# Performance work log

Measured on AMD Instinct MI355X. Metric: run time of the kernel, lower is better.

The kernel has to match this reference:

```python
import jax, jax.numpy as jnp
import numpy as np

B, C, S = 4, 512, 8192   # batch, channels, seq len
E = 256                  # q_dim // r1 = projected dim
D = 256                  # dilaion: block size; window width = 2*D (D even)


def setup_inputs() -> dict:
    key = jax.random.key(0)
    ks = jax.random.split(key, 6)
    w = 0.05
    return {
        "x1": jax.random.normal(ks[0], (B, C, S), jnp.float32),
        "mask": jnp.ones((B, 1, S), jnp.float32),
        "Wq": jax.random.normal(ks[1], (E, C), jnp.float32) * w,
        "bq": jnp.zeros((E,), jnp.float32),
        "Wk": jax.random.normal(ks[2], (E, C), jnp.float32) * w,
        "bk": jnp.zeros((E,), jnp.float32),
        "Wv": jax.random.normal(ks[3], (E, C), jnp.float32) * w,
        "bv": jnp.zeros((E,), jnp.float32),
        "Wo": jax.random.normal(ks[4], (C, E), jnp.float32) * w,
        "bo": jnp.zeros((C,), jnp.float32),
    }


def _windows(x, nb, d):
    # x: [B, ch, S] -> nb overlapping windows of width 2d (stride d, halo d//2 each side)
    b, ch, _ = x.shape
    xp = jnp.pad(x, ((0, 0), (0, 0), (d // 2, d // 2)))  # [B, ch, S + d]
    lo = xp[:, :, : nb * d].reshape(b, ch, nb, d)
    hi = xp[:, :, d:].reshape(b, ch, nb, d)
    return jnp.concatenate([lo, hi], axis=-1).transpose(0, 2, 1, 3)  # [B, nb, ch, 2d]


def reference(x1, mask, Wq, bq, Wk, bk, Wv, bv, Wo, bo):
    nb = S // D  # S divisible by D -> no tail padding branch
    # 1x1 conv projections
    q = jnp.einsum('ec,bcs->bes', Wq, x1) + bq[None, :, None]
    k = jnp.einsum('ec,bcs->bes', Wk, x1) + bk[None, :, None]
    v = jnp.einsum('ec,bcs->bes', Wv, x1) + bv[None, :, None]

    qw = q.reshape(B, E, nb, D).transpose(0, 2, 1, 3)   # [B, nb, E, D]
    kw = _windows(k, nb, D)                              # [B, nb, E, 2D]
    vw = _windows(v, nb, D)                              # [B, nb, E, 2D]
    pm = mask[:, 0:1, :]                                 # padding mask [B,1,S]
    pmw = _windows(pm, nb, D)                            # [B, nb, 1, 2D]

    W = 2 * D
    # original loop `window_mask[:, :, i:i+D] = 1 for i in range(D)` -> union covers
    # columns [0, 2D-2]; only the last column stays 0 (rows identical)
    win = (jnp.arange(W) < W - 1).astype(jnp.float32)    # [2D]
    fmask = win[None, None, None, :] * pmw               # [B, nb, 1, 2D]

    energy = jnp.einsum('bneq,bnek->bnqk', qw, kw) / np.float32(np.sqrt(E))
    attn = jax.nn.softmax(energy + jnp.log(fmask + 1e-6), axis=-1) * fmask
    out = jnp.einsum('bnek,bnqk->bneq', vw, attn)        # [B, nb, E, D]

    h = jax.nn.gelu(out, approximate=False)
    h = jnp.einsum('oe,bneq->bnoq', Wo, h) + bo[None, None, :, None]  # [B, nb, C, D]
    y = h.transpose(0, 2, 1, 3).reshape(B, C, nb * D)[:, :, :S]
    return y * mask[:, 0:1, :]
```

## Files before the change

kernel.cpp:

```cpp
#include <hip/hip_runtime.h>
#include <hip/hip_bf16.h>

typedef __attribute__((ext_vector_type(8))) short short8;
typedef __attribute__((ext_vector_type(4))) float f32x4;
typedef __attribute__((ext_vector_type(4))) int int4v;

#define DI __device__ __forceinline__

constexpr int Bq = 4, Cc = 512, Ss = 8192, Ee = 256;
constexpr int SP = 8448;
constexpr long XSLAB = 4194304;

DI unsigned short f2bf(float f) {
    unsigned int u = __float_as_uint(f);
    unsigned int r = u + 0x7fffu + ((u >> 16) & 1u);
    return (unsigned short)(r >> 16);
}

union U16x8 { int4v v; unsigned short u[8]; };

DI void gll16(const void* g, void* l) {
    __builtin_amdgcn_global_load_lds(
        (const __attribute__((address_space(1))) unsigned int*)g,
        (__attribute__((address_space(3))) unsigned int*)l, 16, 0, 0);
}

DI unsigned pkbf(float lo, float hi) {
    unsigned r;
    asm("v_cvt_pk_bf16_f32 %0, %1, %2" : "=v"(r) : "v"(lo), "v"(hi));
    return r;
}

DI short8 mk8(unsigned a, unsigned b, unsigned c, unsigned d) {
    int4v v; v[0] = (int)a; v[1] = (int)b; v[2] = (int)c; v[3] = (int)d;
    union { int4v i; short8 s; } U; U.i = v; return U.s;
}

DI f32x4 max4(f32x4 a, f32x4 b) {
    f32x4 r;
    r[0] = fmaxf(a[0], b[0]); r[1] = fmaxf(a[1], b[1]);
    r[2] = fmaxf(a[2], b[2]); r[3] = fmaxf(a[3], b[3]);
    return r;
}

DI float gelu_t(float x) {
    float x2 = x * x;
    float z = x * (0.7978845608f + 0.0356774081f * x2);
    float az = fabsf(z);
    float e = __expf(-2.f * az);
    float th = (1.f - e) / (1.f + e);
    th = (z < 0.f) ? -th : th;
    return 0.5f * x * (1.f + th);
}

DI int SIG(int k)  { return ((k & 4) << 2) | ((k & 24) >> 1) | (k & 3); }
DI int SIG2(int k) { return SIG(SIG(k)); }

__global__ __launch_bounds__(256) void kprep(
    const float* __restrict__ Wq, const float* __restrict__ Wk, const float* __restrict__ Wv,
    const float* __restrict__ Wo, unsigned short* __restrict__ Wqkv_b, unsigned short* __restrict__ Wo_b,
    unsigned short* __restrict__ kTp, unsigned short* __restrict__ vp)
{
    int blk = blockIdx.x, t = threadIdx.x;
    if (blk < 1536) {
        int i = blk * 256 + t;
        if (i < 768 * 512) {
            int m = i >> 9, c = i & 511;
            const float* src = (m < 256) ? Wq : ((m < 512) ? Wk : Wv);
            Wqkv_b[i] = f2bf(src[(m & 255) * 512 + c]);
        }
        if (i < 512 * 256) {
            int kap = i & 255;
            int src = (i & ~255) | (kap & ~31) | SIG(kap & 31);
            Wo_b[i] = f2bf(Wo[src]);
        }
    } else {
        int i = (blk - 1536) * 256 + t;
        int4v z = {0, 0, 0, 0};
        if (i < 32768) {
            int b = i >> 13, r = i & 8191;
            int side = r >> 12, off = r & 4095;
            *(int4v*)(kTp + (long)b * SP * 256 + (long)(side ? 8320 : 0) * 256 + off * 8) = z;
        } else {
            int j = i - 32768;
            int b = j >> 13, r = j & 8191;
            int row = r >> 5, side = (r >> 4) & 1, sc = r & 15;
            *(int4v*)(vp + ((long)b * 256 + row) * SP + side * 8320 + sc * 8) = z;
        }
    }
}

__global__ __launch_bounds__(256) void ktr_x(const float* __restrict__ x1g, unsigned short* __restrict__ xT4)
{
    const float* x1b = x1g + (long)blockIdx.y * Cc * Ss;
    unsigned short* xT = xT4 + (long)blockIdx.y * XSLAB;
    __shared__ unsigned short tile[64][72];
    int t = threadIdx.x;
    int bs = blockIdx.x & 127, bc = blockIdx.x >> 7;
    int s0 = bs * 64, c0 = bc * 64;
    int cl = t >> 4, sl = (t & 15) * 4;
    for (int it = 0; it < 4; ++it) {
        int c = cl + it * 16;
        float4 vv = *(const float4*)(x1b + (long)(c0 + c) * Ss + s0 + sl);
        tile[c][sl + 0] = f2bf(vv.x);
        tile[c][sl + 1] = f2bf(vv.y);
        tile[c][sl + 2] = f2bf(vv.z);
        tile[c][sl + 3] = f2bf(vv.w);
    }
    __syncthreads();
    int s_loc = t >> 2, cseg = (t & 3) * 16;
    for (int half = 0; half < 2; ++half) {
        U16x8 u;
        for (int j = 0; j < 8; ++j) u.u[j] = tile[cseg + half * 8 + j][s_loc];
        *(int4v*)(xT + (long)(s0 + s_loc) * Cc + c0 + cseg + half * 8) = u.v;
    }
}

__global__ __launch_bounds__(256) void kqkv(
    const unsigned short* __restrict__ xT4, const unsigned short* __restrict__ Wqkv,
    const float* __restrict__ bq, const float* __restrict__ bk, const float* __restrict__ bv,
    unsigned short* __restrict__ qT, unsigned short* __restrict__ kTp, unsigned short* __restrict__ vp,
    int b0)
{
    __shared__ int4v As[1024], Bs[1024];
    int b = b0 + blockIdx.y;
    const unsigned short* xT = xT4 + (long)blockIdx.y * XSLAB;
    int wg = blockIdx.x;
    int type = wg >> 7, id = wg & 127;
    const unsigned short *A, *Bt; unsigned short* Op;
    long opitch; const float* bias; bool biasRow;
    if (type < 2) {
        int mt = id >> 1, nt = id & 1;
        A  = xT + (long)(mt * 128) * 512;
        Bt = Wqkv + (long)(type * 256 + nt * 128) * 512;
        if (type == 0)
            Op = qT + (long)b * Ss * Ee + (long)(mt * 128) * Ee + nt * 128;
        else
            Op = kTp + (long)b * SP * Ee + (long)(128 + mt * 128) * Ee + nt * 128;
        opitch = Ee;
        bias = (type ? bk : bq) + nt * 128;
        biasRow = false;
    } else {
        int mt = id >> 6, nt = id & 63;
        A  = Wqkv + (long)(512 + mt * 128) * 512;
        Bt = xT + (long)(nt * 128) * 512;
        Op = vp + (long)b * Ee * SP + (long)(mt * 128) * SP + 128 + nt * 128;
        opitch = SP;
        bias = bv + mt * 128;
        biasRow = true;
    }
    int t = threadIdx.x, lane = t & 63, wv = t >> 6;
    int wr = (wv >> 1) * 64, wc = (wv & 1) * 64;

    int soff[4];
    #pragma unroll
    for (int i = 0; i < 4; ++i) {
        int seg = t + 256 * i, row = seg >> 3, cs = seg & 7;
        soff[i] = row * 512 + ((cs ^ (row & 7)) * 8);
    }
    char* adst = (char*)As + wv * 1024;
    char* bdst = (char*)Bs + wv * 1024;

    f32x4 acc[4][4] = {};
    for (int kk = 0; kk < 8; ++kk) {
        #pragma unroll
        for (int i = 0; i < 4; ++i) {
            gll16(A  + soff[i] + kk * 64, adst + i * 4096);
            gll16(Bt + soff[i] + kk * 64, bdst + i * 4096);
        }
        asm volatile("s_waitcnt vmcnt(0)" ::: "memory");
        __syncthreads();
        for (int ks = 0; ks < 2; ++ks) {
            int csk = ks * 4 + (lane >> 4);
            short8 af[4], bfr[4];
            #pragma unroll
            for (int mi = 0; mi < 4; ++mi) {
                int m = wr + mi * 16 + (lane & 15);
                af[mi] = *(const short8*)&As[m * 8 + (csk ^ (m & 7))];
            }
            #pragma unroll
            for (int ni = 0; ni < 4; ++ni) {
                int nn = wc + ni * 16 + (lane & 15);
                bfr[ni] = *(const short8*)&Bs[nn * 8 + (csk ^ (nn & 7))];
            }
            #pragma unroll
            for (int mi = 0; mi < 4; ++mi)
                #pragma unroll
                for (int ni = 0; ni < 4; ++ni)
                    acc[mi][ni] = __builtin_amdgcn_mfma_f32_16x16x32_bf16(af[mi], bfr[ni], acc[mi][ni], 0, 0, 0);
        }
        __syncthreads();
    }
    for (int mi = 0; mi < 4; ++mi)
        for (int ni = 0; ni < 4; ++ni) {
            int mrow = wr + mi * 16 + ((lane >> 4) * 4);
            int ncol = wc + ni * 16 + (lane & 15);
            int nc2 = biasRow ? ((ncol & ~31) | SIG2(ncol & 31)) : ncol;
            for (int r = 0; r < 4; ++r) {
                float bval = biasRow ? bias[mrow + r] : bias[ncol];
                Op[(long)(mrow + r) * opitch + nc2] = f2bf(acc[mi][ni][r] + bval);
            }
        }
}

__global__ __launch_bounds__(512, 1) void kattn(
    const unsigned short* __restrict__ qT, const unsigned short* __restrict__ kTp,
    const unsigned short* __restrict__ vp,  const unsigned short* __restrict__ Wo_b,
    const float* __restrict__ mask, const float* __restrict__ bo,
    float* __restrict__ y)
{
    __shared__ __align__(16) char SH[137216];
    float* fmaskL = (float*)(SH + 131072);
    float* l2maskL = (float*)(SH + 133120);
    float* boL    = (float*)(SH + 135168);

    int t = threadIdx.x, lane = t & 63, wv = t >> 6;
    int G = lane >> 4, l15 = lane & 15;

    int phys = blockIdx.x;
    int xx = phys & 7, kk2 = phys >> 3;
    int L = ((xx + 8 * (kk2 >> 1)) << 1) | (kk2 & 1);
    int qh = L & 1, n = (L >> 1) & 31, b = L >> 6;
    int sqw = n * 256 + qh * 128 + wv * 16;

    short8 qfrag[8];
    #pragma unroll
    for (int s = 0; s < 8; ++s)
        qfrag[s] = *(const short8*)(qT + ((long)b * Ss + sqw + l15) * 256 + 32 * s + 8 * G);

    {
        int i = t;
        int sw = n * 256 - 128 + i;
        float f = 0.f;
        if (i != 511 && sw >= 0 && sw < Ss) f = mask[(long)b * Ss + sw];
        fmaskL[i] = f;
        l2maskL[i] = __log2f(f + 1e-6f);
    }
    if (t < 128) ((float4*)boL)[t] = ((const float4*)bo)[t];

    const unsigned short* ksrcp[4];
    const unsigned short* vsrcp[4];
    #pragma unroll
    for (int i = 0; i < 4; ++i) {
        int krow = wv * 8 + i * 2 + (lane >> 5);
        ksrcp[i] = kTp + ((long)b * SP + n * 256 + krow) * 256 + (((lane & 31) ^ (krow & 7)) * 8);
        int erow = wv * 32 + i * 8 + (lane >> 3);
        vsrcp[i] = vp + ((long)b * 256 + erow) * SP + n * 256 + (((lane & 7) ^ ((lane >> 3) & 7)) * 8);
    }

#define STAGE(CH, BUF) {                                                      \
        char* kl = SH + (BUF) * 32768 + wv * 4096;                            \
        char* vl = SH + 65536 + (BUF) * 32768 + wv * 4096;                    \
        _Pragma("unroll")                                                     \
        for (int i = 0; i < 4; ++i) gll16(ksrcp[i] + (long)(CH) * 16384, kl + i * 1024); \
        _Pragma("unroll")                                                     \
        for (int i = 0; i < 4; ++i) gll16(vsrcp[i] + (CH) * 64, vl + i * 1024);          \
    }

#define QKBLOCK(E, KB) {                                                      \
        __builtin_amdgcn_s_setprio(1);                                        \
        _Pragma("unroll")                                                     \
        for (int s = 0; s < 8; ++s) {                                         \
            short8 kf[4];                                                     \
            _Pragma("unroll")                                                 \
            for (int tt = 0; tt < 4; ++tt)                                    \
                kf[tt] = *(const short8*)((KB) + (16 * tt + l15) * 512 + (((4 * s + G) ^ (l15 & 7)) * 16)); \
            _Pragma("unroll")                                                 \
            for (int tt = 0; tt < 4; ++tt)                                    \
                E[tt] = __builtin_amdgcn_mfma_f32_16x16x32_bf16(kf[tt], qfrag[s], E[tt], 0, 0, 0); \
        }                                                                     \
        __builtin_amdgcn_s_setprio(0);                                        \
    }

    STAGE(0, 0)
    STAGE(1, 1)
    asm volatile("s_waitcnt vmcnt(4) lgkmcnt(0)" ::: "memory");
    __builtin_amdgcn_s_barrier();

    float mrun = -1e30f, lrun = 0.f;
    f32x4 oacc[16] = {};
    f32x4 eC[4] = {}, eN[4] = {};

    QKBLOCK(eC, SH)

    #pragma unroll 2
    for (int ch = 0; ch < 8; ++ch) {
        const char* VB = SH + 65536 + (ch & 1) * 32768;

        if (ch < 7) {
            const char* KBn = SH + ((ch + 1) & 1) * 32768;
            QKBLOCK(eN, KBn)
        }

        int w0 = ch * 64;
        f32x4 lm[4], fm[4];
        #pragma unroll
        for (int tt = 0; tt < 4; ++tt) {
            lm[tt] = *(const f32x4*)&l2maskL[w0 + 16 * tt + 4 * G];
            fm[tt] = *(const f32x4*)&fmaskL[w0 + 16 * tt + 4 * G];
        }

        f32x4 ev[4];
        f32x4 m4;
        #pragma unroll
        for (int tt = 0; tt < 4; ++tt) {
            ev[tt] = eC[tt] * 0.09016844f + lm[tt];
            m4 = tt ? max4(m4, ev[tt]) : ev[tt];
        }
        float cm = fmaxf(fmaxf(m4[0], m4[1]), fmaxf(m4[2], m4[3]));
        cm = fmaxf(cm, __shfl_xor(cm, 16));
        cm = fmaxf(cm, __shfl_xor(cm, 32));
        if (__any(cm > mrun + 11.5416f)) {
            float mn = fmaxf(mrun, cm);
            float sc = exp2f(mrun - mn);
            mrun = mn; lrun *= sc;
            #pragma unroll
            for (int et = 0; et < 16; ++et) oacc[et] *= sc;
        }

        unsigned pc[8];
        float ssum = 0.f;
        #pragma unroll
        for (int tt = 0; tt < 4; ++tt) {
            f32x4 p;
            p[0] = exp2f(ev[tt][0] - mrun);
            p[1] = exp2f(ev[tt][1] - mrun);
            p[2] = exp2f(ev[tt][2] - mrun);
            p[3] = exp2f(ev[tt][3] - mrun);
            ssum += (p[0] + p[1]) + (p[2] + p[3]);
            f32x4 pf = p * fm[tt];
            pc[2 * tt]     = pkbf(pf[0], pf[1]);
            pc[2 * tt + 1] = pkbf(pf[2], pf[3]);
        }
        ssum += __shfl_xor(ssum, 16);
        ssum += __shfl_xor(ssum, 32);
        lrun += ssum;

        __builtin_amdgcn_s_setprio(1);
        #pragma unroll
        for (int s = 0; s < 2; ++s) {
            short8 pf = mk8(pc[4 * s], pc[4 * s + 1], pc[4 * s + 2], pc[4 * s + 3]);
            #pragma unroll
            for (int et = 0; et < 16; ++et) {
                short8 vf = *(const short8*)(VB + (16 * et + l15) * 128 + (((4 * s + G) ^ (l15 & 7)) * 16));
                oacc[et] = __builtin_amdgcn_mfma_f32_16x16x32_bf16(vf, pf, oacc[et], 0, 0, 0);
            }
        }
        __builtin_amdgcn_s_setprio(0);

        asm volatile("s_waitcnt lgkmcnt(0)" ::: "memory");
        __builtin_amdgcn_s_barrier();
        if (ch < 6) {
            STAGE(ch + 2, ch & 1)
            asm volatile("s_waitcnt vmcnt(4)" ::: "memory");
        } else if (ch == 6) {
            asm volatile("s_waitcnt vmcnt(0)" ::: "memory");
        }
        __builtin_amdgcn_s_barrier();

        #pragma unroll
        for (int tt = 0; tt < 4; ++tt) { eC[tt] = eN[tt]; eN[tt] = (f32x4){}; }
    }

    float linv = 1.f / lrun;
    unsigned hc[32];
    #pragma unroll
    for (int et = 0; et < 16; ++et) {
        f32x4 xv = oacc[et] * linv;
        hc[2 * et]     = pkbf(gelu_t(xv[0]), gelu_t(xv[1]));
        hc[2 * et + 1] = pkbf(gelu_t(xv[2]), gelu_t(xv[3]));
    }
    float ym = fmaskL[128 + qh * 128 + wv * 16 + l15];

    const unsigned short* wsrcp[4];
    #pragma unroll
    for (int i = 0; i < 4; ++i) {
        int wrow = wv * 8 + i * 2 + (lane >> 5);
        wsrcp[i] = Wo_b + (long)wrow * 256 + (((lane & 31) ^ (wrow & 7)) * 8);
    }
#define WSTAGE(ST, BUF) {                                                     \
        char* wl = SH + (BUF) * 32768 + wv * 4096;                            \
        _Pragma("unroll")                                                     \
        for (int i = 0; i < 4; ++i) gll16(wsrcp[i] + (ST) * 16384, wl + i * 1024); \
    }

    WSTAGE(0, 0)
    WSTAGE(1, 1)
    asm volatile("s_waitcnt vmcnt(4)" ::: "memory");
    __builtin_amdgcn_s_barrier();

    for (int step = 0; step < 8; ++step) {
        const char* WB = SH + (step & 1) * 32768;
        __builtin_amdgcn_s_setprio(1);
        #pragma unroll
        for (int otl = 0; otl < 4; ++otl) {
            f32x4 pacc = {};
            #pragma unroll
            for (int s = 0; s < 8; ++s) {
                short8 wf = *(const short8*)(WB + (16 * otl + l15) * 512 + (((4 * s + G) ^ (l15 & 7)) * 16));
                short8 hs = mk8(hc[4 * s], hc[4 * s + 1], hc[4 * s + 2], hc[4 * s + 3]);
                pacc = __builtin_amdgcn_mfma_f32_16x16x32_bf16(wf, hs, pacc, 0, 0, 0);
            }
            int o0 = step * 64 + 16 * otl + 4 * G;
            f32x4 bo4 = *(const f32x4*)&boL[o0];
            #pragma unroll
            for (int r = 0; r < 4; ++r)
                y[((long)b * Cc + o0 + r) * Ss + sqw + l15] = (pacc[r] + bo4[r]) * ym;
        }
        __builtin_amdgcn_s_setprio(0);
        asm volatile("s_waitcnt lgkmcnt(0)" ::: "memory");
        __builtin_amdgcn_s_barrier();
        if (step < 6) {
            WSTAGE(step + 2, step & 1)
            asm volatile("s_waitcnt vmcnt(4)" ::: "memory");
        } else if (step == 6) {
            asm volatile("s_waitcnt vmcnt(0)" ::: "memory");
        }
        __builtin_amdgcn_s_barrier();
    }
#undef STAGE
#undef WSTAGE
#undef QKBLOCK
}

extern "C" void kernel_launch(void* const* d_in, const int* in_sizes, int n_in,
                              void* d_out, int out_size, void* d_ws, size_t ws_size,
                              hipStream_t stream)
{
    const float* x1   = (const float*)d_in[0];
    const float* mask = (const float*)d_in[1];
    const float* Wq   = (const float*)d_in[2];
    const float* bq   = (const float*)d_in[3];
    const float* Wk   = (const float*)d_in[4];
    const float* bk   = (const float*)d_in[5];
    const float* Wv   = (const float*)d_in[6];
    const float* bv   = (const float*)d_in[7];
    const float* Wo   = (const float*)d_in[8];
    const float* bo   = (const float*)d_in[9];
    float* y = (float*)d_out;

    if (ws_size < 60817408u) return;
    char* w = (char*)d_ws;
    unsigned short* Wqkv_b = (unsigned short*)(w);
    unsigned short* Wo_b   = (unsigned short*)(w + 786432);
    unsigned short* qT     = (unsigned short*)(w + 1048576);
    unsigned short* kTp    = (unsigned short*)(w + 17825792);
    unsigned short* vp     = (unsigned short*)(w + 35127296);
    unsigned short* xT4    = (unsigned short*)(w + 52428800);

    int g = (int)((ws_size - 52428800u) / 8388608u);
    if (g < 1) g = 1;
    if (g > 4) g = 4;

    kprep<<<1792, 256, 0, stream>>>(Wq, Wk, Wv, Wo, Wqkv_b, Wo_b, kTp, vp);
    for (int b0 = 0; b0 < 4; b0 += g) {
        int gy = (4 - b0 < g) ? (4 - b0) : g;
        ktr_x<<<dim3(1024, gy), 256, 0, stream>>>(x1 + (long)b0 * Cc * Ss, xT4);
        kqkv<<<dim3(384, gy), 256, 0, stream>>>(xT4, Wqkv_b, bq, bk, bv, qT, kTp, vp, b0);
    }
    kattn<<<256, 512, 0, stream>>>(qT, kTp, vp, Wo_b, mask, bo, y);
}
```

Baseline: 122.8 us.

## Split attention blocks to 4 waves with smaller K/V chunks for 2 blocks/CU

Restructures the attention kernel from 512-thread blocks covering 128 queries to 256-thread blocks covering 64 queries, launching 512 blocks with launch bounds allowing two per CU. K/V and Wo are now staged in 32-key and 32-output chunks (16 iterations), which halves LDS use so two blocks can share a CU. It also drops the software-pipelined QK computation (computing next chunk's energy during the current one) in favour of a simple in-loop QK. The intent is to hide latency through more resident waves and better load balance. The cost is twice the K/V/Wo global traffic per query and more barrier iterations.

```diff
diff --git a/kernel.cpp b/kernel.cpp
--- a/kernel.cpp
+++ b/kernel.cpp
@@ -203,33 +203,31 @@
         }
 }
 
-__global__ __launch_bounds__(512, 1) void kattn(
+__global__ __launch_bounds__(256, 2) void kattn(
     const unsigned short* __restrict__ qT, const unsigned short* __restrict__ kTp,
     const unsigned short* __restrict__ vp,  const unsigned short* __restrict__ Wo_b,
     const float* __restrict__ mask, const float* __restrict__ bo,
     float* __restrict__ y)
 {
-    __shared__ __align__(16) char SH[137216];
-    float* fmaskL = (float*)(SH + 131072);
-    float* l2maskL = (float*)(SH + 133120);
-    float* boL    = (float*)(SH + 135168);
+    __shared__ __align__(16) char SH[71680];
+    float* fmaskL  = (float*)(SH + 65536);
+    float* l2maskL = (float*)(SH + 67584);
+    float* boL     = (float*)(SH + 69632);
 
     int t = threadIdx.x, lane = t & 63, wv = t >> 6;
     int G = lane >> 4, l15 = lane & 15;
 
     int phys = blockIdx.x;
-    int xx = phys & 7, kk2 = phys >> 3;
-    int L = ((xx + 8 * (kk2 >> 1)) << 1) | (kk2 & 1);
-    int qh = L & 1, n = (L >> 1) & 31, b = L >> 6;
-    int sqw = n * 256 + qh * 128 + wv * 16;
+    int L = (phys & 7) * 64 + (phys >> 3);
+    int qq = L & 3, n = (L >> 2) & 31, b = L >> 7;
+    int sqw = n * 256 + qq * 64 + wv * 16;
 
     short8 qfrag[8];
     #pragma unroll
     for (int s = 0; s < 8; ++s)
         qfrag[s] = *(const short8*)(qT + ((long)b * Ss + sqw + l15) * 256 + 32 * s + 8 * G);
 
-    {
-        int i = t;
+    for (int i = t; i < 512; i += 256) {
         int sw = n * 256 - 128 + i;
         float f = 0.f;
         if (i != 511 && sw >= 0 && sw < Ss) f = mask[(long)b * Ss + sw];
@@ -244,32 +242,17 @@
     for (int i = 0; i < 4; ++i) {
         int krow = wv * 8 + i * 2 + (lane >> 5);
         ksrcp[i] = kTp + ((long)b * SP + n * 256 + krow) * 256 + (((lane & 31) ^ (krow & 7)) * 8);
-        int erow = wv * 32 + i * 8 + (lane >> 3);
-        vsrcp[i] = vp + ((long)b * 256 + erow) * SP + n * 256 + (((lane & 7) ^ ((lane >> 3) & 7)) * 8);
+        int erow = wv * 64 + i * 16 + (lane >> 2);
+        vsrcp[i] = vp + ((long)b * 256 + erow) * SP + n * 256 + (((lane & 3) ^ ((lane >> 2) & 3)) * 8);
     }
 
 #define STAGE(CH, BUF) {                                                      \
-        char* kl = SH + (BUF) * 32768 + wv * 4096;                            \
-        char* vl = SH + 65536 + (BUF) * 32768 + wv * 4096;                    \
+        char* kl = SH + (BUF) * 16384 + wv * 4096;                            \
+        char* vl = SH + 32768 + (BUF) * 16384 + wv * 4096;                    \
         _Pragma("unroll")                                                     \
-        for (int i = 0; i < 4; ++i) gll16(ksrcp[i] + (long)(CH) * 16384, kl + i * 1024); \
+        for (int i = 0; i < 4; ++i) gll16(ksrcp[i] + (long)(CH) * 8192, kl + i * 1024); \
         _Pragma("unroll")                                                     \
-        for (int i = 0; i < 4; ++i) gll16(vsrcp[i] + (CH) * 64, vl + i * 1024);          \
-    }
-
-#define QKBLOCK(E, KB) {                                                      \
-        __builtin_amdgcn_s_setprio(1);                                        \
-        _Pragma("unroll")                                                     \
-        for (int s = 0; s < 8; ++s) {                                         \
-            short8 kf[4];                                                     \
-            _Pragma("unroll")                                                 \
-            for (int tt = 0; tt < 4; ++tt)                                    \
-                kf[tt] = *(const short8*)((KB) + (16 * tt + l15) * 512 + (((4 * s + G) ^ (l15 & 7)) * 16)); \
-            _Pragma("unroll")                                                 \
-            for (int tt = 0; tt < 4; ++tt)                                    \
-                E[tt] = __builtin_amdgcn_mfma_f32_16x16x32_bf16(kf[tt], qfrag[s], E[tt], 0, 0, 0); \
-        }                                                                     \
-        __builtin_amdgcn_s_setprio(0);                                        \
+        for (int i = 0; i < 4; ++i) gll16(vsrcp[i] + (CH) * 32, vl + i * 1024);          \
     }
 
     STAGE(0, 0)
@@ -279,34 +262,39 @@
 
     float mrun = -1e30f, lrun = 0.f;
     f32x4 oacc[16] = {};
-    f32x4 eC[4] = {}, eN[4] = {};
-
-    QKBLOCK(eC, SH)
 
     #pragma unroll 2
-    for (int ch = 0; ch < 8; ++ch) {
-        const char* VB = SH + 65536 + (ch & 1) * 32768;
-
-        if (ch < 7) {
-            const char* KBn = SH + ((ch + 1) & 1) * 32768;
-            QKBLOCK(eN, KBn)
-        }
-
-        int w0 = ch * 64;
-        f32x4 lm[4], fm[4];
-        #pragma unroll
-        for (int tt = 0; tt < 4; ++tt) {
+    for (int ch = 0; ch < 16; ++ch) {
+        const char* KB = SH + (ch & 1) * 16384;
+        const char* VB = SH + 32768 + (ch & 1) * 16384;
+
+        f32x4 eacc[2] = {};
+        __builtin_amdgcn_s_setprio(1);
+        #pragma unroll
+        for (int s = 0; s < 8; ++s) {
+            short8 kf[2];
+            #pragma unroll
+            for (int tt = 0; tt < 2; ++tt)
+                kf[tt] = *(const short8*)(KB + (16 * tt + l15) * 512 + (((4 * s + G) ^ (l15 & 7)) * 16));
+            #pragma unroll
+            for (int tt = 0; tt < 2; ++tt)
+                eacc[tt] = __builtin_amdgcn_mfma_f32_16x16x32_bf16(kf[tt], qfrag[s], eacc[tt], 0, 0, 0);
+        }
+        __builtin_amdgcn_s_setprio(0);
+
+        int w0 = ch * 32;
+        f32x4 lm[2], fm[2];
+        #pragma unroll
+        for (int tt = 0; tt < 2; ++tt) {
             lm[tt] = *(const f32x4*)&l2maskL[w0 + 16 * tt + 4 * G];
             fm[tt] = *(const f32x4*)&fmaskL[w0 + 16 * tt + 4 * G];
         }
 
-        f32x4 ev[4];
-        f32x4 m4;
-        #pragma unroll
-        for (int tt = 0; tt < 4; ++tt) {
-            ev[tt] = eC[tt] * 0.09016844f + lm[tt];
-            m4 = tt ? max4(m4, ev[tt]) : ev[tt];
-        }
+        f32x4 ev[2];
+        #pragma unroll
+        for (int tt = 0; tt < 2; ++tt)
+            ev[tt] = eacc[tt] * 0.09016844f + lm[tt];
+        f32x4 m4 = max4(ev[0], ev[1]);
         float cm = fmaxf(fmaxf(m4[0], m4[1]), fmaxf(m4[2], m4[3]));
         cm = fmaxf(cm, __shfl_xor(cm, 16));
         cm = fmaxf(cm, __shfl_xor(cm, 32));
@@ -318,10 +306,10 @@
             for (int et = 0; et < 16; ++et) oacc[et] *= sc;
         }
 
-        unsigned pc[8];
+        unsigned pc[4];
         float ssum = 0.f;
         #pragma unroll
-        for (int tt = 0; tt < 4; ++tt) {
+        for (int tt = 0; tt < 2; ++tt) {
             f32x4 p;
             p[0] = exp2f(ev[tt][0] - mrun);
             p[1] = exp2f(ev[tt][1] - mrun);
@@ -337,12 +325,11 @@
         lrun += ssum;
 
         __builtin_amdgcn_s_setprio(1);
-        #pragma unroll
-        for (int s = 0; s < 2; ++s) {
-            short8 pf = mk8(pc[4 * s], pc[4 * s + 1], pc[4 * s + 2], pc[4 * s + 3]);
+        {
+            short8 pf = mk8(pc[0], pc[1], pc[2], pc[3]);
             #pragma unroll
             for (int et = 0; et < 16; ++et) {
-                short8 vf = *(const short8*)(VB + (16 * et + l15) * 128 + (((4 * s + G) ^ (l15 & 7)) * 16));
+                short8 vf = *(const short8*)(VB + (16 * et + l15) * 64 + ((G ^ (l15 & 3)) * 16));
                 oacc[et] = __builtin_amdgcn_mfma_f32_16x16x32_bf16(vf, pf, oacc[et], 0, 0, 0);
             }
         }
@@ -350,16 +337,13 @@
 
         asm volatile("s_waitcnt lgkmcnt(0)" ::: "memory");
         __builtin_amdgcn_s_barrier();
-        if (ch < 6) {
+        if (ch < 14) {
             STAGE(ch + 2, ch & 1)
             asm volatile("s_waitcnt vmcnt(4)" ::: "memory");
-        } else if (ch == 6) {
+        } else if (ch == 14) {
             asm volatile("s_waitcnt vmcnt(0)" ::: "memory");
         }
         __builtin_amdgcn_s_barrier();
-
-        #pragma unroll
-        for (int tt = 0; tt < 4; ++tt) { eC[tt] = eN[tt]; eN[tt] = (f32x4){}; }
     }
 
     float linv = 1.f / lrun;
@@ -370,7 +354,7 @@
         hc[2 * et]     = pkbf(gelu_t(xv[0]), gelu_t(xv[1]));
         hc[2 * et + 1] = pkbf(gelu_t(xv[2]), gelu_t(xv[3]));
     }
-    float ym = fmaskL[128 + qh * 128 + wv * 16 + l15];
+    float ym = fmaskL[128 + qq * 64 + wv * 16 + l15];
 
     const unsigned short* wsrcp[4];
     #pragma unroll
@@ -379,9 +363,9 @@
         wsrcp[i] = Wo_b + (long)wrow * 256 + (((lane & 31) ^ (wrow & 7)) * 8);
     }
 #define WSTAGE(ST, BUF) {                                                     \
-        char* wl = SH + (BUF) * 32768 + wv * 4096;                            \
+        char* wl = SH + (BUF) * 16384 + wv * 4096;                            \
         _Pragma("unroll")                                                     \
-        for (int i = 0; i < 4; ++i) gll16(wsrcp[i] + (ST) * 16384, wl + i * 1024); \
+        for (int i = 0; i < 4; ++i) gll16(wsrcp[i] + (ST) * 8192, wl + i * 1024); \
     }
 
     WSTAGE(0, 0)
@@ -389,11 +373,12 @@
     asm volatile("s_waitcnt vmcnt(4)" ::: "memory");
     __builtin_amdgcn_s_barrier();
 
-    for (int step = 0; step < 8; ++step) {
-        const char* WB = SH + (step & 1) * 32768;
+    #pragma unroll 2
+    for (int step = 0; step < 16; ++step) {
+        const char* WB = SH + (step & 1) * 16384;
         __builtin_amdgcn_s_setprio(1);
         #pragma unroll
-        for (int otl = 0; otl < 4; ++otl) {
+        for (int otl = 0; otl < 2; ++otl) {
             f32x4 pacc = {};
             #pragma unroll
             for (int s = 0; s < 8; ++s) {
@@ -401,7 +386,7 @@
                 short8 hs = mk8(hc[4 * s], hc[4 * s + 1], hc[4 * s + 2], hc[4 * s + 3]);
                 pacc = __builtin_amdgcn_mfma_f32_16x16x32_bf16(wf, hs, pacc, 0, 0, 0);
             }
-            int o0 = step * 64 + 16 * otl + 4 * G;
+            int o0 = step * 32 + 16 * otl + 4 * G;
             f32x4 bo4 = *(const f32x4*)&boL[o0];
             #pragma unroll
             for (int r = 0; r < 4; ++r)
@@ -410,17 +395,16 @@
         __builtin_amdgcn_s_setprio(0);
         asm volatile("s_waitcnt lgkmcnt(0)" ::: "memory");
         __builtin_amdgcn_s_barrier();
-        if (step < 6) {
+        if (step < 14) {
             WSTAGE(step + 2, step & 1)
             asm volatile("s_waitcnt vmcnt(4)" ::: "memory");
-        } else if (step == 6) {
+        } else if (step == 14) {
             asm volatile("s_waitcnt vmcnt(0)" ::: "memory");
         }
         __builtin_amdgcn_s_barrier();
     }
 #undef STAGE
 #undef WSTAGE
-#undef QKBLOCK
 }
 
 extern "C" void kernel_launch(void* const* d_in, const int* in_sizes, int n_in,
@@ -458,5 +442,5 @@
         ktr_x<<<dim3(1024, gy), 256, 0, stream>>>(x1 + (long)b0 * Cc * Ss, xT4);
         kqkv<<<dim3(384, gy), 256, 0, stream>>>(xT4, Wqkv_b, bq, bk, bv, qT, kTp, vp, b0);
     }
-    kattn<<<256, 512, 0, stream>>>(qT, kTp, vp, Wo_b, mask, bo, y);
-}
+    kattn<<<512, 256, 0, stream>>>(qT, kTp, vp, Wo_b, mask, bo, y);
+}
```

Result: no change. 123.6 us (+0.7%).
